# Kernel tuning notes

Measured on AMD Instinct MI355X. Metric: run time of the kernel, lower is better.

The kernel has to match this reference:

```python
import jax, jax.numpy as jnp
import numpy as np

NDIM = 2
NSIG = 2
NCELLS = 1000
BATCH = 4
DT = 1e-3
NSTEPS = 251  # 1 + int((t1 - t0)/dt) with t0=0, t1=0.25
SIGMA = 1e-3


def _phi(y, pw1, pb1, pw2, pb2, pw3, pb3, pw4, pb4, pw5, pb5):
    # phi_nn: 2 -> 16 -> 32 -> 32 -> 16 -> 1 with tanh activations
    h = jnp.tanh(y @ pw1.T + pb1)
    h = jnp.tanh(h @ pw2.T + pb2)
    h = jnp.tanh(h @ pw3.T + pb3)
    h = jnp.tanh(h @ pw4.T + pb4)
    return h @ pw5.T + pb5  # (ncells, 1)


def setup_inputs() -> dict:
    key = jax.random.key(0)
    ks = jax.random.split(key, 16)
    # x = [t0, t1, y0.flat, tcrit, p0(2), p1(2)] per batch item
    y0 = 0.1 * jax.random.normal(ks[0], (BATCH, NCELLS, NDIM), dtype=jnp.float32)
    t0 = jnp.zeros((BATCH, 1), jnp.float32)
    t1 = jnp.full((BATCH, 1), 0.25, jnp.float32)
    tcrit = jnp.full((BATCH, 1), 0.125, jnp.float32)
    p0 = jax.random.normal(ks[1], (BATCH, 2), dtype=jnp.float32)
    p1 = jax.random.normal(ks[2], (BATCH, 2), dtype=jnp.float32)
    x = jnp.concatenate([t0, t1, y0.reshape(BATCH, -1), tcrit, p0, p1], axis=1)
    # Wiener increments ~ N(0, dt)
    dw = np.sqrt(DT).astype(np.float32) * jax.random.normal(
        ks[3], (BATCH, NSTEPS, NCELLS, NDIM), dtype=jnp.float32)
    # phi_nn weights (torch Linear: weight is (out, in)), init N(0, 0.1), bias 0
    def w(k, o, i):
        return 0.1 * jax.random.normal(k, (o, i), dtype=jnp.float32)
    inp = dict(x=x, dw=dw,
               pw1=w(ks[4], 16, 2), pb1=jnp.zeros(16, jnp.float32),
               pw2=w(ks[5], 32, 16), pb2=jnp.zeros(32, jnp.float32),
               pw3=w(ks[6], 32, 32), pb3=jnp.zeros(32, jnp.float32),
               pw4=w(ks[7], 16, 32), pb4=jnp.zeros(16, jnp.float32),
               pw5=w(ks[8], 1, 16), pb5=jnp.zeros(1, jnp.float32),
               tw=w(ks[9], NDIM, NSIG), tb=jnp.zeros(NDIM, jnp.float32))
    return inp


def reference(x, dw, pw1, pb1, pw2, pb2, pw3, pb3, pw4, pb4, pw5, pb5, tw, tb):
    phi_params = (pw1, pb1, pw2, pb2, pw3, pb3, pw4, pb4, pw5, pb5)
    grad_phi = jax.grad(lambda yy: jnp.sum(_phi(yy, *phi_params)))

    def simulate(xi, dwi):
        t0 = xi[0]
        y0 = xi[2:2 + NCELLS * NDIM].reshape(NCELLS, NDIM)
        ps = xi[2 + NCELLS * NDIM:]
        tcrit, p0, p1 = ps[0], ps[1:3], ps[3:5]
        ts = t0 + DT * jnp.arange(NSTEPS, dtype=xi.dtype)

        def step(y, t_dw):
            t, dwt = t_dw
            sig = jnp.where(t < tcrit, p0, p1)      # step signal f_signal(t, params)
            tilt = sig @ tw.T + tb                  # grad_tilt: (ndim,)
            drift = -(grad_phi(y) + tilt)           # f(t, y)
            y_new = y + drift * DT + SIGMA * dwt    # Euler-Maruyama
            return y_new, None

        y_final, _ = jax.lax.scan(step, y0, (ts, dwi))
        return y_final

    return jax.vmap(simulate)(x, dw)  # (BATCH, NCELLS, NDIM)
```

## Files before the change

### kernel.cpp

```cpp
#include <hip/hip_runtime.h>

#define NDIMC 2
#define NCELLS 1000
#define BATCHSZ 4
#define NSTEPS 251
#define XROW 2007

__device__ __forceinline__ float fast_tanh(float x) {
    float e = __builtin_amdgcn_exp2f(x * 2.885390081777926774f);
    float r = __builtin_amdgcn_rcpf(e + 1.0f);
    return fmaf(-2.0f, r, 1.0f);
}

#define LDS_FENCE() asm volatile("s_waitcnt lgkmcnt(0)" ::: "memory")

__device__ __forceinline__ void pkfma(float2& a, float2 w, float2 v) {
    asm("v_pk_fma_f32 %0, %1, %2, %0" : "+v"(a) : "v"(w), "v"(v));
}
__device__ __forceinline__ float2 pkadd(float2 a, float2 b) {
    float2 r;
    asm("v_pk_add_f32 %0, %1, %2" : "=v"(r) : "v"(a), "v"(b));
    return r;
}

template<int CTRL>
__device__ __forceinline__ float dpp_xor_add(float z) {
    int t = __builtin_amdgcn_update_dpp(0, __float_as_int(z), CTRL, 0xf, 0xf, true);
    return z + __int_as_float(t);
}
__device__ __forceinline__ float row16_sum(float z) {
    z = dpp_xor_add<0xB1>(z);
    z = dpp_xor_add<0x1B>(z);
    z = dpp_xor_add<0x141>(z);
    z = dpp_xor_add<0x140>(z);
    return z;
}

__device__ __forceinline__ float pdot16(const float2 (&w)[8], const float* lds,
                                        float bias) {
    const float4 v0 = *(const float4*)(lds + 0);
    const float4 v1 = *(const float4*)(lds + 4);
    const float4 v2 = *(const float4*)(lds + 8);
    const float4 v3 = *(const float4*)(lds + 12);
    float2 a0 = make_float2(bias, 0.f), a1 = make_float2(0.f, 0.f);
    float2 a2 = make_float2(0.f, 0.f),  a3 = make_float2(0.f, 0.f);
    pkfma(a0, w[0], make_float2(v0.x, v0.y)); pkfma(a1, w[1], make_float2(v0.z, v0.w));
    pkfma(a2, w[2], make_float2(v1.x, v1.y)); pkfma(a3, w[3], make_float2(v1.z, v1.w));
    pkfma(a0, w[4], make_float2(v2.x, v2.y)); pkfma(a1, w[5], make_float2(v2.z, v2.w));
    pkfma(a2, w[6], make_float2(v3.x, v3.y)); pkfma(a3, w[7], make_float2(v3.z, v3.w));
    float2 s = pkadd(pkadd(a0, a1), pkadd(a2, a3));
    return s.x + s.y;
}

__device__ __forceinline__ float pdot32(const float2 (&w)[16], const float* lds,
                                        float bias) {
    float2 a0 = make_float2(bias, 0.f), a1 = make_float2(0.f, 0.f);
    float2 a2 = make_float2(0.f, 0.f),  a3 = make_float2(0.f, 0.f);
    #pragma unroll
    for (int c = 0; c < 2; ++c) {
        const float4 u0 = *(const float4*)(lds + c * 16 + 0);
        const float4 u1 = *(const float4*)(lds + c * 16 + 4);
        const float4 u2 = *(const float4*)(lds + c * 16 + 8);
        const float4 u3 = *(const float4*)(lds + c * 16 + 12);
        pkfma(a0, w[c*8+0], make_float2(u0.x, u0.y));
        pkfma(a1, w[c*8+1], make_float2(u0.z, u0.w));
        pkfma(a2, w[c*8+2], make_float2(u1.x, u1.y));
        pkfma(a3, w[c*8+3], make_float2(u1.z, u1.w));
        pkfma(a0, w[c*8+4], make_float2(u2.x, u2.y));
        pkfma(a1, w[c*8+5], make_float2(u2.z, u2.w));
        pkfma(a2, w[c*8+6], make_float2(u3.x, u3.y));
        pkfma(a3, w[c*8+7], make_float2(u3.z, u3.w));
    }
    float2 s = pkadd(pkadd(a0, a1), pkadd(a2, a3));
    return s.x + s.y;
}

__global__ __launch_bounds__(64, 2)
void phinn_sde_kernel(const float* __restrict__ x,   const float* __restrict__ dw,
                      const float* __restrict__ pw1, const float* __restrict__ pb1,
                      const float* __restrict__ pw2, const float* __restrict__ pb2,
                      const float* __restrict__ pw3, const float* __restrict__ pb3,
                      const float* __restrict__ pw4, const float* __restrict__ pb4,
                      const float* __restrict__ pw5, const float* __restrict__ pb5,
                      const float* __restrict__ tw,  const float* __restrict__ tb,
                      float* __restrict__ out)
{
    __shared__ float sh[2][6][32];

    const int tid  = threadIdx.x;
    const int n    = tid & 31;
    const int grp  = tid >> 5;
    const int s16  = n & 15;
    const int b    = blockIdx.x / (NCELLS / 2);
    const int pair = blockIdx.x % (NCELLS / 2);
    const int cell = pair * 2 + grp;

    const float r1a = pw1[s16 * 2 + 0];
    const float r1b = pw1[s16 * 2 + 1];
    const float rb1 = pb1[s16];

    float2 w2p[8];
    #pragma unroll
    for (int j = 0; j < 8; ++j) w2p[j] = ((const float2*)pw2)[n * 8 + j];
    const float rb2 = pb2[n];

    float2 w3p[16];
    #pragma unroll
    for (int j = 0; j < 16; ++j) w3p[j] = ((const float2*)pw3)[n * 16 + j];
    const float rb3 = pb3[n];

    float2 w4p[16];
    #pragma unroll
    for (int j = 0; j < 16; ++j) w4p[j] = ((const float2*)pw4)[s16 * 16 + j];
    const float rb4 = pb4[s16];

    const float rw5 = pw5[s16];

    float2 w4cp[8];
    #pragma unroll
    for (int j = 0; j < 8; ++j)
        w4cp[j] = make_float2(pw4[(2*j) * 32 + n], pw4[(2*j+1) * 32 + n]);

    float2 w3cp[16];
    #pragma unroll
    for (int j = 0; j < 16; ++j)
        w3cp[j] = make_float2(pw3[(2*j) * 32 + n], pw3[(2*j+1) * 32 + n]);

    float2 w2cp[16];
    #pragma unroll
    for (int j = 0; j < 16; ++j)
        w2cp[j] = make_float2(pw2[(2*j) * 16 + s16], pw2[(2*j+1) * 16 + s16]);

    const float* xb = x + (size_t)b * XROW;
    const float t0v    = xb[0];
    const float tcritv = xb[2 + NCELLS * NDIMC];
    const float p0x = xb[2003], p0y = xb[2004];
    const float p1x = xb[2005], p1y = xb[2006];
    const float tA0 = fmaf(p0x, tw[0], fmaf(p0y, tw[1], tb[0]));
    const float tA1 = fmaf(p0x, tw[2], fmaf(p0y, tw[3], tb[1]));
    const float tB0 = fmaf(p1x, tw[0], fmaf(p1y, tw[1], tb[0]));
    const float tB1 = fmaf(p1x, tw[2], fmaf(p1y, tw[3], tb[1]));

    float y0 = xb[2 + cell * 2 + 0];
    float y1 = xb[2 + cell * 2 + 1];

    const float* dwb = dw + (size_t)b * NSTEPS * NCELLS * NDIMC
                          + (size_t)pair * 2 * NDIMC;
    int dwoff = grp * NDIMC;

    const float* l0 = &sh[grp][0][0];
    const float* l1 = &sh[grp][1][0];
    const float* l2 = &sh[grp][2][0];
    const float* l3 = &sh[grp][3][0];
    const float* l4 = &sh[grp][4][0];
    const float* l5 = &sh[grp][5][0];

    #pragma unroll 1
    for (int i = 0; i < NSTEPS; ++i) {
        const float2 dwv = *(const float2*)(dwb + dwoff);
        dwoff += NCELLS * NDIMC;
        const float t = t0v + 0.001f * (float)i;

        const float h1 = fast_tanh(fmaf(r1a, y0, fmaf(r1b, y1, rb1)));
        sh[grp][0][n] = h1;
        LDS_FENCE();

        const float h2 = fast_tanh(pdot16(w2p, l0, rb2));
        sh[grp][1][n] = h2;
        LDS_FENCE();

        const float h3 = fast_tanh(pdot32(w3p, l1, rb3));
        sh[grp][2][n] = h3;
        LDS_FENCE();

        const float h4 = fast_tanh(pdot32(w4p, l2, rb4));

        const float g4p = rw5 * fmaf(-h4, h4, 1.0f);
        sh[grp][3][n] = g4p;
        LDS_FENCE();

        const float g3p = pdot16(w4cp, l3, 0.f) * fmaf(-h3, h3, 1.0f);
        sh[grp][4][n] = g3p;
        LDS_FENCE();

        const float g2p = pdot32(w3cp, l4, 0.f) * fmaf(-h2, h2, 1.0f);
        sh[grp][5][n] = g2p;
        LDS_FENCE();

        const float g1p = pdot32(w2cp, l5, 0.f) * fmaf(-h1, h1, 1.0f);

        const float v0 = row16_sum(r1a * g1p);
        const float v1 = row16_sum(r1b * g1p);

        const bool  cnd   = t < tcritv;
        const float tilt0 = cnd ? tA0 : tB0;
        const float tilt1 = cnd ? tA1 : tB1;
        y0 = fmaf(-0.001f, v0 + tilt0, fmaf(0.001f, dwv.x, y0));
        y1 = fmaf(-0.001f, v1 + tilt1, fmaf(0.001f, dwv.y, y1));
    }

    if (n == 0) {
        *(float2*)(out + ((size_t)b * NCELLS + cell) * NDIMC) = make_float2(y0, y1);
    }
}

extern "C" void kernel_launch(void* const* d_in, const int* in_sizes, int n_in,
                              void* d_out, int out_size, void* d_ws, size_t ws_size,
                              hipStream_t stream) {
    const float* x   = (const float*)d_in[0];
    const float* dw  = (const float*)d_in[1];
    const float* pw1 = (const float*)d_in[2];
    const float* pb1 = (const float*)d_in[3];
    const float* pw2 = (const float*)d_in[4];
    const float* pb2 = (const float*)d_in[5];
    const float* pw3 = (const float*)d_in[6];
    const float* pb3 = (const float*)d_in[7];
    const float* pw4 = (const float*)d_in[8];
    const float* pb4 = (const float*)d_in[9];
    const float* pw5 = (const float*)d_in[10];
    const float* pb5 = (const float*)d_in[11];
    const float* tw  = (const float*)d_in[12];
    const float* tb  = (const float*)d_in[13];
    float* out = (float*)d_out;

    dim3 grid(BATCHSZ * NCELLS / 2);
    dim3 block(64);
    phinn_sde_kernel<<<grid, block, 0, stream>>>(x, dw, pw1, pb1, pw2, pb2,
                                                 pw3, pb3, pw4, pb4, pw5, pb5,
                                                 tw, tb, out);
}
```

Measured before the change: 296.2 us.

## Replace LDS activation exchange with DPP gathers and permlane16 swaps

```diff
diff --git a/kernel.cpp b/kernel.cpp
--- a/kernel.cpp
+++ b/kernel.cpp
@@ -12,8 +12,6 @@
     return fmaf(-2.0f, r, 1.0f);
 }
 
-#define LDS_FENCE() asm volatile("s_waitcnt lgkmcnt(0)" ::: "memory")
-
 __device__ __forceinline__ void pkfma(float2& a, float2 w, float2 v) {
     asm("v_pk_fma_f32 %0, %1, %2, %0" : "+v"(a) : "v"(w), "v"(v));
 }
@@ -24,53 +22,58 @@
 }
 
 template<int CTRL>
-__device__ __forceinline__ float dpp_xor_add(float z) {
-    int t = __builtin_amdgcn_update_dpp(0, __float_as_int(z), CTRL, 0xf, 0xf, true);
-    return z + __int_as_float(t);
+__device__ __forceinline__ float dpp_mov(float x) {
+    return __int_as_float(__builtin_amdgcn_update_dpp(
+        0, __float_as_int(x), CTRL, 0xf, 0xf, true));
+}
+template<int CTRL>
+__device__ __forceinline__ float dpp_add(float z) {
+    return z + dpp_mov<CTRL>(z);
 }
 __device__ __forceinline__ float row16_sum(float z) {
-    z = dpp_xor_add<0xB1>(z);
-    z = dpp_xor_add<0x1B>(z);
-    z = dpp_xor_add<0x141>(z);
-    z = dpp_xor_add<0x140>(z);
+    z = dpp_add<0xB1>(z);
+    z = dpp_add<0x1B>(z);
+    z = dpp_add<0x141>(z);
+    z = dpp_add<0x140>(z);
     return z;
 }
 
-__device__ __forceinline__ float pdot16(const float2 (&w)[8], const float* lds,
-                                        float bias) {
-    const float4 v0 = *(const float4*)(lds + 0);
-    const float4 v1 = *(const float4*)(lds + 4);
-    const float4 v2 = *(const float4*)(lds + 8);
-    const float4 v3 = *(const float4*)(lds + 12);
+__device__ __forceinline__ float xor16(float z, bool odd) {
+    float t = z, u = z;
+    asm("v_permlane16_swap_b32 %0, %1" : "+v"(t), "+v"(u));
+    return odd ? t : u;
+}
+
+struct G16 { float2 p[8]; };
+__device__ __forceinline__ G16 gather16(float z) {
+    G16 g;
+    const float v0 = z;
+    const float v1 = dpp_mov<0x4E>(v0);
+    const float v2 = dpp_mov<0x141>(v0);
+    const float v3 = dpp_mov<0x141>(v1);
+    const float v4 = dpp_mov<0x140>(v0);
+    const float v5 = dpp_mov<0x140>(v1);
+    const float v6 = dpp_mov<0x140>(v2);
+    const float v7 = dpp_mov<0x140>(v3);
+    g.p[0] = make_float2(v0, dpp_mov<0xB1>(v0));
+    g.p[1] = make_float2(v1, dpp_mov<0xB1>(v1));
+    g.p[2] = make_float2(v2, dpp_mov<0xB1>(v2));
+    g.p[3] = make_float2(v3, dpp_mov<0xB1>(v3));
+    g.p[4] = make_float2(v4, dpp_mov<0xB1>(v4));
+    g.p[5] = make_float2(v5, dpp_mov<0xB1>(v5));
+    g.p[6] = make_float2(v6, dpp_mov<0xB1>(v6));
+    g.p[7] = make_float2(v7, dpp_mov<0xB1>(v7));
+    return g;
+}
+
+__device__ __forceinline__ float pdot8(const float2 (&w)[8], const G16& g,
+                                       float bias) {
     float2 a0 = make_float2(bias, 0.f), a1 = make_float2(0.f, 0.f);
     float2 a2 = make_float2(0.f, 0.f),  a3 = make_float2(0.f, 0.f);
-    pkfma(a0, w[0], make_float2(v0.x, v0.y)); pkfma(a1, w[1], make_float2(v0.z, v0.w));
-    pkfma(a2, w[2], make_float2(v1.x, v1.y)); pkfma(a3, w[3], make_float2(v1.z, v1.w));
-    pkfma(a0, w[4], make_float2(v2.x, v2.y)); pkfma(a1, w[5], make_float2(v2.z, v2.w));
-    pkfma(a2, w[6], make_float2(v3.x, v3.y)); pkfma(a3, w[7], make_float2(v3.z, v3.w));
-    float2 s = pkadd(pkadd(a0, a1), pkadd(a2, a3));
-    return s.x + s.y;
-}
-
-__device__ __forceinline__ float pdot32(const float2 (&w)[16], const float* lds,
-                                        float bias) {
-    float2 a0 = make_float2(bias, 0.f), a1 = make_float2(0.f, 0.f);
-    float2 a2 = make_float2(0.f, 0.f),  a3 = make_float2(0.f, 0.f);
-    #pragma unroll
-    for (int c = 0; c < 2; ++c) {
-        const float4 u0 = *(const float4*)(lds + c * 16 + 0);
-        const float4 u1 = *(const float4*)(lds + c * 16 + 4);
-        const float4 u2 = *(const float4*)(lds + c * 16 + 8);
-        const float4 u3 = *(const float4*)(lds + c * 16 + 12);
-        pkfma(a0, w[c*8+0], make_float2(u0.x, u0.y));
-        pkfma(a1, w[c*8+1], make_float2(u0.z, u0.w));
-        pkfma(a2, w[c*8+2], make_float2(u1.x, u1.y));
-        pkfma(a3, w[c*8+3], make_float2(u1.z, u1.w));
-        pkfma(a0, w[c*8+4], make_float2(u2.x, u2.y));
-        pkfma(a1, w[c*8+5], make_float2(u2.z, u2.w));
-        pkfma(a2, w[c*8+6], make_float2(u3.x, u3.y));
-        pkfma(a3, w[c*8+7], make_float2(u3.z, u3.w));
-    }
+    pkfma(a0, w[0], g.p[0]); pkfma(a1, w[1], g.p[1]);
+    pkfma(a2, w[2], g.p[2]); pkfma(a3, w[3], g.p[3]);
+    pkfma(a0, w[4], g.p[4]); pkfma(a1, w[5], g.p[5]);
+    pkfma(a2, w[6], g.p[6]); pkfma(a3, w[7], g.p[7]);
     float2 s = pkadd(pkadd(a0, a1), pkadd(a2, a3));
     return s.x + s.y;
 }
@@ -85,51 +88,44 @@
                       const float* __restrict__ tw,  const float* __restrict__ tb,
                       float* __restrict__ out)
 {
-    __shared__ float sh[2][6][32];
-
     const int tid  = threadIdx.x;
     const int n    = tid & 31;
+    const int l    = n & 15;
+    const int s16  = l;
+    const int np   = n ^ 16;
+    const int rbk  = (n >> 4) * 16;
+    const bool odd = (tid >> 4) & 1;
     const int grp  = tid >> 5;
-    const int s16  = n & 15;
     const int b    = blockIdx.x / (NCELLS / 2);
     const int pair = blockIdx.x % (NCELLS / 2);
     const int cell = pair * 2 + grp;
 
+    const int TAU[8] = {0, 2, 7, 5, 15, 13, 8, 10};
+
     const float r1a = pw1[s16 * 2 + 0];
     const float r1b = pw1[s16 * 2 + 1];
     const float rb1 = pb1[s16];
-
-    float2 w2p[8];
+    const float rb2 = pb2[n];
+    const float rb3 = pb3[n];
+    const float rb4 = pb4[s16];
+    const float rw5 = pw5[s16];
+
+    float2 w2f[8], w3P[8], w3Q[8], w4f[8], w4b[8], w3bP[8], w3bQ[8], w2b[8];
     #pragma unroll
-    for (int j = 0; j < 8; ++j) w2p[j] = ((const float2*)pw2)[n * 8 + j];
-    const float rb2 = pb2[n];
-
-    float2 w3p[16];
-    #pragma unroll
-    for (int j = 0; j < 16; ++j) w3p[j] = ((const float2*)pw3)[n * 16 + j];
-    const float rb3 = pb3[n];
-
-    float2 w4p[16];
-    #pragma unroll
-    for (int j = 0; j < 16; ++j) w4p[j] = ((const float2*)pw4)[s16 * 16 + j];
-    const float rb4 = pb4[s16];
-
-    const float rw5 = pw5[s16];
-
-    float2 w4cp[8];
-    #pragma unroll
-    for (int j = 0; j < 8; ++j)
-        w4cp[j] = make_float2(pw4[(2*j) * 32 + n], pw4[(2*j+1) * 32 + n]);
-
-    float2 w3cp[16];
-    #pragma unroll
-    for (int j = 0; j < 16; ++j)
-        w3cp[j] = make_float2(pw3[(2*j) * 32 + n], pw3[(2*j+1) * 32 + n]);
-
-    float2 w2cp[16];
-    #pragma unroll
-    for (int j = 0; j < 16; ++j)
-        w2cp[j] = make_float2(pw2[(2*j) * 16 + s16], pw2[(2*j+1) * 16 + s16]);
+    for (int t = 0; t < 8; ++t) {
+        const int j0 = l ^ TAU[t];
+        const int j1 = j0 ^ 1;
+        const int k0 = rbk + j0;
+        const int k1 = rbk + j1;
+        w2f[t]  = make_float2(pw2[n * 16 + j0],   pw2[n * 16 + j1]);
+        w3P[t]  = make_float2(pw3[n * 32 + k0],   pw3[n * 32 + k1]);
+        w3Q[t]  = make_float2(pw3[np * 32 + k0],  pw3[np * 32 + k1]);
+        w4f[t]  = make_float2(pw4[s16 * 32 + k0], pw4[s16 * 32 + k1]);
+        w4b[t]  = make_float2(pw4[j0 * 32 + n],   pw4[j1 * 32 + n]);
+        w3bP[t] = make_float2(pw3[k0 * 32 + n],   pw3[k1 * 32 + n]);
+        w3bQ[t] = make_float2(pw3[k0 * 32 + np],  pw3[k1 * 32 + np]);
+        w2b[t]  = make_float2(pw2[k0 * 16 + s16], pw2[k1 * 16 + s16]);
+    }
 
     const float* xb = x + (size_t)b * XROW;
     const float t0v    = xb[0];
@@ -148,13 +144,6 @@
                           + (size_t)pair * 2 * NDIMC;
     int dwoff = grp * NDIMC;
 
-    const float* l0 = &sh[grp][0][0];
-    const float* l1 = &sh[grp][1][0];
-    const float* l2 = &sh[grp][2][0];
-    const float* l3 = &sh[grp][3][0];
-    const float* l4 = &sh[grp][4][0];
-    const float* l5 = &sh[grp][5][0];
-
     #pragma unroll 1
     for (int i = 0; i < NSTEPS; ++i) {
         const float2 dwv = *(const float2*)(dwb + dwoff);
@@ -162,32 +151,31 @@
         const float t = t0v + 0.001f * (float)i;
 
         const float h1 = fast_tanh(fmaf(r1a, y0, fmaf(r1b, y1, rb1)));
-        sh[grp][0][n] = h1;
-        LDS_FENCE();
-
-        const float h2 = fast_tanh(pdot16(w2p, l0, rb2));
-        sh[grp][1][n] = h2;
-        LDS_FENCE();
-
-        const float h3 = fast_tanh(pdot32(w3p, l1, rb3));
-        sh[grp][2][n] = h3;
-        LDS_FENCE();
-
-        const float h4 = fast_tanh(pdot32(w4p, l2, rb4));
+
+        const G16 g1v = gather16(h1);
+        const float h2 = fast_tanh(pdot8(w2f, g1v, rb2));
+
+        const G16 g2v = gather16(h2);
+        const float h3 = fast_tanh(pdot8(w3P, g2v, rb3)
+                                   + xor16(pdot8(w3Q, g2v, 0.f), odd));
+
+        const G16 g3v = gather16(h3);
+        const float A4 = pdot8(w4f, g3v, 0.f);
+        const float h4 = fast_tanh(A4 + xor16(A4, odd) + rb4);
 
         const float g4p = rw5 * fmaf(-h4, h4, 1.0f);
-        sh[grp][3][n] = g4p;
-        LDS_FENCE();
-
-        const float g3p = pdot16(w4cp, l3, 0.f) * fmaf(-h3, h3, 1.0f);
-        sh[grp][4][n] = g3p;
-        LDS_FENCE();
-
-        const float g2p = pdot32(w3cp, l4, 0.f) * fmaf(-h2, h2, 1.0f);
-        sh[grp][5][n] = g2p;
-        LDS_FENCE();
-
-        const float g1p = pdot32(w2cp, l5, 0.f) * fmaf(-h1, h1, 1.0f);
+
+        const G16 g4v = gather16(g4p);
+        const float g3p = pdot8(w4b, g4v, 0.f) * fmaf(-h3, h3, 1.0f);
+
+        const G16 g5v = gather16(g3p);
+        const float g2p = (pdot8(w3bP, g5v, 0.f)
+                           + xor16(pdot8(w3bQ, g5v, 0.f), odd))
+                          * fmaf(-h2, h2, 1.0f);
+
+        const G16 g6v = gather16(g2p);
+        const float A1 = pdot8(w2b, g6v, 0.f);
+        const float g1p = (A1 + xor16(A1, odd)) * fmaf(-h1, h1, 1.0f);
 
         const float v0 = row16_sum(r1a * g1p);
         const float v1 = row16_sum(r1b * g1p);
```

New measurement: 329.8 us. +11.3%, slower.
